# Performance work log

Hardware: AMD Instinct MI355X
Metric: run time of the kernel (lower is better)

Reference implementation:

```python
import jax, jax.numpy as jnp
import numpy as np


def setup_inputs() -> dict:
    key = jax.random.key(0)
    ks = jax.random.split(key, 9)
    B, S, I, H, O = 64, 2048, 256, 256, 256
    s_g = 1.0 / np.sqrt(I + H)  # torch Linear default init scale
    s_f = 1.0 / np.sqrt(H)
    return {
        "x": jax.random.normal(ks[0], (B, S, I), dtype=jnp.float32),
        "W_r": jax.random.normal(ks[1], (H, I + H), dtype=jnp.float32) * s_g,
        "b_r": jax.random.normal(ks[2], (H,), dtype=jnp.float32) * s_g,
        "W_z": jax.random.normal(ks[3], (H, I + H), dtype=jnp.float32) * s_g,
        "b_z": jax.random.normal(ks[4], (H,), dtype=jnp.float32) * s_g,
        "W_h": jax.random.normal(ks[5], (H, I + H), dtype=jnp.float32) * s_g,
        "b_h": jax.random.normal(ks[6], (H,), dtype=jnp.float32) * s_g,
        "W_fc": jax.random.normal(ks[7], (O, H), dtype=jnp.float32) * s_f,
        "b_fc": jax.random.normal(ks[8], (O,), dtype=jnp.float32) * s_f,
    }


def reference(x, W_r, b_r, W_z, b_z, W_h, b_h, W_fc, b_fc):
    B, S, I = x.shape
    H = W_r.shape[0]
    h0 = jnp.zeros((B, H), dtype=x.dtype)

    def step(h, x_t):
        comb = jnp.concatenate([x_t, h], axis=1)            # [B, I+H]
        r = jax.nn.sigmoid(comb @ W_r.T + b_r)              # reset gate
        z = jax.nn.sigmoid(comb @ W_z.T + b_z)              # update gate
        comb_r = jnp.concatenate([x_t, r * h], axis=1)
        h_tilde = jnp.tanh(comb_r @ W_h.T + b_h)
        h_new = (1.0 - z) * h + z * h_tilde
        return h_new, h_new

    # scan over time (strict sequential dependency), x as [S, B, I]
    h_last, hs = jax.lax.scan(step, h0, jnp.swapaxes(x, 0, 1))
    outputs = jnp.einsum('sbh,oh->bso', hs, W_fc) + b_fc    # [B, S, O]
    return outputs, h_last
```

## Files before the change

### kernel.cpp

```cpp
#include <hip/hip_runtime.h>
#include <hip/hip_bf16.h>
#include <hip/hip_fp16.h>

typedef unsigned short u16;
typedef unsigned int u32;
typedef __attribute__((ext_vector_type(8))) short bf16x8;
typedef __attribute__((ext_vector_type(4))) float f32x4;
typedef _Float16 __attribute__((ext_vector_type(2))) f16x2;

#define MFMA16(a, b, c) __builtin_amdgcn_mfma_f32_16x16x32_bf16((a), (b), (c), 0, 0, 0)

__device__ __forceinline__ float bflo(u32 u) { return __uint_as_float(u << 16); }
__device__ __forceinline__ float bfhi(u32 u) { return __uint_as_float(u & 0xffff0000u); }
__device__ __forceinline__ float bf1(u16 u) { return __uint_as_float(((u32)u) << 16); }
__device__ __forceinline__ u16 f2bf(float f) {
    __hip_bfloat16 b = __float2bfloat16(f);
    return __builtin_bit_cast(u16, b);
}

__device__ __forceinline__ int sniff_fp32(const void* Wr) {
    const uint4* p = (const uint4*)Wr;
    uint4 v = p[threadIdx.x & 15];
    u32 a[4] = {v.x, v.y, v.z, v.w};
    float m = 0.f;
#pragma unroll
    for (int i = 0; i < 4; ++i) {
        float lo = fabsf(bflo(a[i])), hi = fabsf(bfhi(a[i]));
        if (!(lo < 1e30f)) lo = 1e30f;
        if (!(hi < 1e30f)) hi = 1e30f;
        m = fmaxf(m, fmaxf(lo, hi));
    }
#pragma unroll
    for (int off = 32; off; off >>= 1) m = fmaxf(m, __shfl_xor(m, off, 64));
    return m > 100.f ? 1 : 0;
}

__device__ __forceinline__ bf16x8 load8bf(const void* base, size_t idx, int f32) {
    if (f32) {
        const float4* p = (const float4*)((const float*)base + idx);
        float4 v0 = p[0], v1 = p[1];
        bf16x8 r;
        r[0] = (short)f2bf(v0.x); r[1] = (short)f2bf(v0.y);
        r[2] = (short)f2bf(v0.z); r[3] = (short)f2bf(v0.w);
        r[4] = (short)f2bf(v1.x); r[5] = (short)f2bf(v1.y);
        r[6] = (short)f2bf(v1.z); r[7] = (short)f2bf(v1.w);
        return r;
    }
    return *(const bf16x8*)((const u16*)base + idx);
}

__device__ __forceinline__ void load8h(const void* base, size_t idx, int f32, f16x2* dst) {
    if (f32) {
        const float4* p = (const float4*)((const float*)base + idx);
        float4 v0 = p[0], v1 = p[1];
        dst[0] = f16x2{(_Float16)v0.x, (_Float16)v0.y};
        dst[1] = f16x2{(_Float16)v0.z, (_Float16)v0.w};
        dst[2] = f16x2{(_Float16)v1.x, (_Float16)v1.y};
        dst[3] = f16x2{(_Float16)v1.z, (_Float16)v1.w};
    } else {
        uint4 v = *(const uint4*)((const u16*)base + idx);
        dst[0] = f16x2{(_Float16)bflo(v.x), (_Float16)bfhi(v.x)};
        dst[1] = f16x2{(_Float16)bflo(v.y), (_Float16)bfhi(v.y)};
        dst[2] = f16x2{(_Float16)bflo(v.z), (_Float16)bfhi(v.z)};
        dst[3] = f16x2{(_Float16)bflo(v.w), (_Float16)bfhi(v.w)};
    }
}

__device__ __forceinline__ float load1f(const void* base, size_t idx, int f32) {
    return f32 ? ((const float*)base)[idx] : bf1(((const u16*)base)[idx]);
}

__global__ __launch_bounds__(256) void gru_pre(
    const void* __restrict__ x,
    const void* __restrict__ Wr, const void* __restrict__ Wz, const void* __restrict__ Wh,
    const void* __restrict__ br, const void* __restrict__ bz, const void* __restrict__ bh,
    __half* __restrict__ gxc, int s0, int lgSc)
{
    const int f32 = sniff_fp32(Wr);
    const int lane = threadIdx.x & 63;
    const int wave = threadIdx.x >> 6;
    const int q = lane >> 4, l16 = lane & 15;
    const int m0 = blockIdx.x * 64 + wave * 16;
    const int by = blockIdx.y;
    const int g = by >> 2;
    const int out0 = (by & 3) * 64;
    const void* W    = (g == 0) ? Wr : ((g == 1) ? Wz : Wh);
    const void* bias = (g == 0) ? br : ((g == 1) ? bz : bh);
    const int Sc = 1 << lgSc;

    const int mA = m0 + l16;
    const int bA = mA >> lgSc;
    const int slA = mA & (Sc - 1);
    const size_t aidx = ((size_t)(bA * 2048 + s0 + slA)) * 256 + q * 8;
    const size_t widx = (size_t)(out0 + l16) * 512 + q * 8;

    f32x4 acc[4] = {{0,0,0,0},{0,0,0,0},{0,0,0,0},{0,0,0,0}};
#pragma unroll
    for (int k0 = 0; k0 < 256; k0 += 32) {
        bf16x8 af = load8bf(x, aidx + k0, f32);
#pragma unroll
        for (int t = 0; t < 4; ++t) {
            bf16x8 bfg = load8bf(W, widx + (size_t)t * 16 * 512 + k0, f32);
            acc[t] = MFMA16(af, bfg, acc[t]);
        }
    }
#pragma unroll
    for (int t = 0; t < 4; ++t) {
        const int col = out0 + t * 16 + l16;
        const float bv = load1f(bias, col, f32);
#pragma unroll
        for (int r = 0; r < 4; ++r) {
            const int row = m0 + q * 4 + r;
            gxc[(size_t)row * 768 + g * 256 + col] = __float2half(acc[t][r] + bv);
        }
    }
}

__device__ __forceinline__ float dot256(const f16x2* w, const _Float16* hp) {
    const uint4* hp4 = (const uint4*)hp;
    float a0 = 0.f, a1 = 0.f, a2 = 0.f, a3 = 0.f;
#pragma unroll
    for (int c = 0; c < 32; ++c) {
        uint4 hv = hp4[c];
        f16x2 h0 = __builtin_bit_cast(f16x2, hv.x);
        f16x2 h1 = __builtin_bit_cast(f16x2, hv.y);
        f16x2 h2 = __builtin_bit_cast(f16x2, hv.z);
        f16x2 h3 = __builtin_bit_cast(f16x2, hv.w);
#if __has_builtin(__builtin_amdgcn_fdot2)
        a0 = __builtin_amdgcn_fdot2(w[c * 4 + 0], h0, a0, false);
        a1 = __builtin_amdgcn_fdot2(w[c * 4 + 1], h1, a1, false);
        a2 = __builtin_amdgcn_fdot2(w[c * 4 + 2], h2, a2, false);
        a3 = __builtin_amdgcn_fdot2(w[c * 4 + 3], h3, a3, false);
#else
        a0 += (float)w[c*4+0][0] * (float)h0[0] + (float)w[c*4+0][1] * (float)h0[1];
        a1 += (float)w[c*4+1][0] * (float)h1[0] + (float)w[c*4+1][1] * (float)h1[1];
        a2 += (float)w[c*4+2][0] * (float)h2[0] + (float)w[c*4+2][1] * (float)h2[1];
        a3 += (float)w[c*4+3][0] * (float)h3[0] + (float)w[c*4+3][1] * (float)h3[1];
#endif
    }
    return (a0 + a1) + (a2 + a3);
}

__global__ __launch_bounds__(768) void gru_scan(
    const __half* __restrict__ gxc,
    const void* __restrict__ Wr, const void* __restrict__ Wz, const void* __restrict__ Wh,
    float* __restrict__ h_state,
    void* __restrict__ outbase,
    int s0, int Sc, int first, int last)
{
    const int f32 = sniff_fp32(Wr);
    const int b = blockIdx.x;
    const int tid = threadIdx.x;
    const int g = tid >> 8;
    const int n = tid & 255;

    __shared__ __align__(16) _Float16 h_h[256];
    __shared__ __align__(16) _Float16 rh_h[256];
    __shared__ float h_f[256];
    __shared__ float z_f[256];

    const void* W = (g == 0) ? Wr : ((g == 1) ? Wz : Wh);
    f16x2 w[128];
#pragma unroll
    for (int c = 0; c < 32; ++c)
        load8h(W, (size_t)n * 512 + 256 + c * 8, f32, &w[c * 4]);

    if (g == 0) {
        float h0 = first ? 0.0f : h_state[b * 256 + n];
        h_f[n] = h0;
        h_h[n] = (_Float16)h0;
    }
    __syncthreads();

    const __half* gxp = gxc + (size_t)b * Sc * 768 + g * 256 + n;
    __half cur = gxp[0];

    for (int s = 0; s < Sc; ++s) {
        __half nxt = (s + 1 < Sc) ? gxp[(size_t)(s + 1) * 768] : cur;

        if (g < 2) {
            float acc = dot256(w, h_h);
            float pre = acc + __half2float(cur);
            pre = fminf(fmaxf(pre, -30.0f), 30.0f);
            float val = __fdividef(1.0f, 1.0f + __expf(-pre));
            if (g == 0) rh_h[n] = (_Float16)(val * h_f[n]);
            else        z_f[n] = val;
        }
        __syncthreads();

        if (g == 2) {
            float acc = dot256(w, rh_h);
            float pre = acc + __half2float(cur);
            pre = fminf(fmaxf(pre, -15.0f), 15.0f);
            float e = __expf(2.0f * pre);
            float ht = __fdividef(e - 1.0f, e + 1.0f);
            float hold = h_f[n];
            float zz = z_f[n];
            float hn = hold + zz * (ht - hold);
            h_f[n] = hn;
            h_h[n] = (_Float16)hn;
            const size_t oidx = (size_t)(b * 2048 + s0 + s) * 256 + n;
            if (f32) ((float*)outbase)[oidx] = hn;
            else     ((u16*)outbase)[oidx] = f2bf(hn);
            if (s == Sc - 1) {
                h_state[b * 256 + n] = hn;
                if (last) {
                    const size_t lidx = (size_t)33554432 + b * 256 + n;
                    if (f32) ((float*)outbase)[lidx] = hn;
                    else     ((u16*)outbase)[lidx] = f2bf(hn);
                }
            }
        }
        __syncthreads();
        cur = nxt;
    }
}

__global__ __launch_bounds__(256) void gru_proj(
    const void* __restrict__ Wfc, const void* __restrict__ bfc,
    const void* __restrict__ Wr_for_sniff,
    void* __restrict__ io)
{
    const int f32 = sniff_fp32(Wr_for_sniff);
    const int lane = threadIdx.x & 63;
    const int wave = threadIdx.x >> 6;
    const int q = lane >> 4, l16 = lane & 15;
    const int m0 = blockIdx.x * 64 + wave * 16;
    const size_t aidx = (size_t)(m0 + l16) * 256 + q * 8;
    const size_t widx = (size_t)l16 * 256 + q * 8;
    f32x4 acc[16];
#pragma unroll
    for (int t = 0; t < 16; ++t) acc[t] = (f32x4){0, 0, 0, 0};
#pragma unroll 2
    for (int k0 = 0; k0 < 256; k0 += 32) {
        bf16x8 af = load8bf(io, aidx + k0, f32);
#pragma unroll
        for (int t = 0; t < 16; ++t) {
            bf16x8 bfg = load8bf(Wfc, widx + (size_t)t * 16 * 256 + k0, f32);
            acc[t] = MFMA16(af, bfg, acc[t]);
        }
    }
#pragma unroll
    for (int t = 0; t < 16; ++t) {
        const int col = t * 16 + l16;
        const float bv = load1f(bfc, col, f32);
#pragma unroll
        for (int r = 0; r < 4; ++r) {
            const size_t oidx = (size_t)(m0 + q * 4 + r) * 256 + col;
            float v = acc[t][r] + bv;
            if (f32) ((float*)io)[oidx] = v;
            else     ((u16*)io)[oidx] = f2bf(v);
        }
    }
}

extern "C" void kernel_launch(void* const* d_in, const int* in_sizes, int n_in,
                              void* d_out, int out_size, void* d_ws, size_t ws_size,
                              hipStream_t stream) {
    (void)in_sizes; (void)n_in; (void)out_size;
    const void* x   = d_in[0];
    const void* Wr  = d_in[1];
    const void* br  = d_in[2];
    const void* Wz  = d_in[3];
    const void* bz  = d_in[4];
    const void* Wh  = d_in[5];
    const void* bh  = d_in[6];
    const void* Wfc = d_in[7];
    const void* bfc = d_in[8];

    float* h_state = (float*)d_ws;
    __half* gxc = (__half*)((char*)d_ws + 65536);

    int lgSc = 11;
    while (lgSc > 0 &&
           (size_t)65536 + (((size_t)64 << lgSc) * 768 * 2) > ws_size) --lgSc;
    const int Sc = 1 << lgSc;

    for (int s0 = 0; s0 < 2048; s0 += Sc) {
        dim3 gpre(Sc, 12);
        gru_pre<<<gpre, 256, 0, stream>>>(x, Wr, Wz, Wh, br, bz, bh, gxc, s0, lgSc);
        gru_scan<<<64, 768, 0, stream>>>(gxc, Wr, Wz, Wh, h_state, d_out,
                                         s0, Sc, (s0 == 0) ? 1 : 0,
                                         (s0 + Sc == 2048) ? 1 : 0);
    }
    gru_proj<<<2048, 256, 0, stream>>>(Wfc, bfc, Wr, d_out);
}
```

Baseline: 4.658 ms.

## Stage x tile in LDS and compute all gate columns per block in gru_pre

gru_pre now loads a 64-row x tile once into shared memory, converting it to bf16, and each block computes all 768 gate outputs. Each wave covers three 64-column tiles with a 4x4 MFMA register tile, and the grid shrinks from Sc×12 to Sc blocks. This removes the 12-fold re-read and re-conversion of x from global memory and improves weight-fragment reuse across M tiles. Launch bounds with minimum-blocks hints are added to both gru_pre and gru_scan. The gru_scan hint could cap its registers and cause spills of its register-held weight slice, even though only 64 blocks launch.

```diff
diff --git a/kernel.cpp b/kernel.cpp
--- a/kernel.cpp
+++ b/kernel.cpp
@@ -70,48 +70,90 @@
     return f32 ? ((const float*)base)[idx] : bf1(((const u16*)base)[idx]);
 }
 
-__global__ __launch_bounds__(256) void gru_pre(
+__global__ __launch_bounds__(256, 2) void gru_pre(
     const void* __restrict__ x,
     const void* __restrict__ Wr, const void* __restrict__ Wz, const void* __restrict__ Wh,
     const void* __restrict__ br, const void* __restrict__ bz, const void* __restrict__ bh,
     __half* __restrict__ gxc, int s0, int lgSc)
 {
     const int f32 = sniff_fp32(Wr);
-    const int lane = threadIdx.x & 63;
-    const int wave = threadIdx.x >> 6;
+    const int tid = threadIdx.x;
+    const int R0 = blockIdx.x * 64;
+
+    __shared__ __align__(16) u16 As[64][264];
+
+    {
+        const int i = tid >> 2;
+        const int kq = (tid & 3) * 64;
+        const int m = R0 + i;
+        const int b = m >> lgSc;
+        const int sl = m & ((1 << lgSc) - 1);
+        const size_t xbase = ((size_t)(b * 2048 + s0 + sl)) * 256 + kq;
+        u16* dst = &As[i][kq];
+        if (f32) {
+            const float4* p = (const float4*)((const float*)x + xbase);
+#pragma unroll
+            for (int j = 0; j < 8; ++j) {
+                float4 v0 = p[2 * j], v1 = p[2 * j + 1];
+                uint4 o;
+                o.x = ((u32)f2bf(v0.y) << 16) | f2bf(v0.x);
+                o.y = ((u32)f2bf(v0.w) << 16) | f2bf(v0.z);
+                o.z = ((u32)f2bf(v1.y) << 16) | f2bf(v1.x);
+                o.w = ((u32)f2bf(v1.w) << 16) | f2bf(v1.z);
+                *(uint4*)(dst + j * 8) = o;
+            }
+        } else {
+            const uint4* p = (const uint4*)((const u16*)x + xbase);
+#pragma unroll
+            for (int j = 0; j < 8; ++j) *(uint4*)(dst + j * 8) = p[j];
+        }
+    }
+    __syncthreads();
+
+    const int wv = tid >> 6;
+    const int lane = tid & 63;
     const int q = lane >> 4, l16 = lane & 15;
-    const int m0 = blockIdx.x * 64 + wave * 16;
-    const int by = blockIdx.y;
-    const int g = by >> 2;
-    const int out0 = (by & 3) * 64;
-    const void* W    = (g == 0) ? Wr : ((g == 1) ? Wz : Wh);
-    const void* bias = (g == 0) ? br : ((g == 1) ? bz : bh);
-    const int Sc = 1 << lgSc;
-
-    const int mA = m0 + l16;
-    const int bA = mA >> lgSc;
-    const int slA = mA & (Sc - 1);
-    const size_t aidx = ((size_t)(bA * 2048 + s0 + slA)) * 256 + q * 8;
-    const size_t widx = (size_t)(out0 + l16) * 512 + q * 8;
-
-    f32x4 acc[4] = {{0,0,0,0},{0,0,0,0},{0,0,0,0},{0,0,0,0}};
-#pragma unroll
-    for (int k0 = 0; k0 < 256; k0 += 32) {
-        bf16x8 af = load8bf(x, aidx + k0, f32);
-#pragma unroll
-        for (int t = 0; t < 4; ++t) {
-            bf16x8 bfg = load8bf(W, widx + (size_t)t * 16 * 512 + k0, f32);
-            acc[t] = MFMA16(af, bfg, acc[t]);
-        }
-    }
-#pragma unroll
-    for (int t = 0; t < 4; ++t) {
-        const int col = out0 + t * 16 + l16;
-        const float bv = load1f(bias, col, f32);
-#pragma unroll
-        for (int r = 0; r < 4; ++r) {
-            const int row = m0 + q * 4 + r;
-            gxc[(size_t)row * 768 + g * 256 + col] = __float2half(acc[t][r] + bv);
+
+    for (int j = 0; j < 3; ++j) {
+        const int gi = wv * 3 + j;
+        const int g = gi >> 2;
+        const int col0 = (gi & 3) * 64;
+        const void* W    = (g == 0) ? Wr : ((g == 1) ? Wz : Wh);
+        const void* bias = (g == 0) ? br : ((g == 1) ? bz : bh);
+        const size_t wbase = (size_t)(col0 + l16) * 512 + q * 8;
+
+        f32x4 acc[4][4];
+#pragma unroll
+        for (int mt = 0; mt < 4; ++mt)
+#pragma unroll
+            for (int nt = 0; nt < 4; ++nt) acc[mt][nt] = (f32x4){0, 0, 0, 0};
+
+#pragma unroll
+        for (int k0 = 0; k0 < 256; k0 += 32) {
+            bf16x8 bfr[4];
+#pragma unroll
+            for (int nt = 0; nt < 4; ++nt)
+                bfr[nt] = load8bf(W, wbase + (size_t)nt * 16 * 512 + k0, f32);
+#pragma unroll
+            for (int mt = 0; mt < 4; ++mt) {
+                bf16x8 af = *(const bf16x8*)&As[mt * 16 + l16][k0 + q * 8];
+#pragma unroll
+                for (int nt = 0; nt < 4; ++nt)
+                    acc[mt][nt] = MFMA16(af, bfr[nt], acc[mt][nt]);
+            }
+        }
+#pragma unroll
+        for (int nt = 0; nt < 4; ++nt) {
+            const int col = col0 + nt * 16 + l16;
+            const float bv = load1f(bias, col, f32);
+#pragma unroll
+            for (int mt = 0; mt < 4; ++mt)
+#pragma unroll
+                for (int r = 0; r < 4; ++r) {
+                    const int row = R0 + mt * 16 + q * 4 + r;
+                    gxc[(size_t)row * 768 + g * 256 + col] =
+                        __float2half(acc[mt][nt][r] + bv);
+                }
         }
     }
 }
@@ -141,7 +183,7 @@
     return (a0 + a1) + (a2 + a3);
 }
 
-__global__ __launch_bounds__(768) void gru_scan(
+__global__ __launch_bounds__(768, 3) void gru_scan(
     const __half* __restrict__ gxc,
     const void* __restrict__ Wr, const void* __restrict__ Wz, const void* __restrict__ Wh,
     float* __restrict__ h_state,
@@ -277,8 +319,7 @@
     const int Sc = 1 << lgSc;
 
     for (int s0 = 0; s0 < 2048; s0 += Sc) {
-        dim3 gpre(Sc, 12);
-        gru_pre<<<gpre, 256, 0, stream>>>(x, Wr, Wz, Wh, br, bz, bh, gxc, s0, lgSc);
+        gru_pre<<<Sc, 256, 0, stream>>>(x, Wr, Wz, Wh, br, bz, bh, gxc, s0, lgSc);
         gru_scan<<<64, 768, 0, stream>>>(gxc, Wr, Wz, Wh, h_state, d_out,
                                          s0, Sc, (s0 == 0) ? 1 : 0,
                                          (s0 + Sc == 2048) ? 1 : 0);
```

New measurement: 4.136 ms. 11.2% less time.
